# Kernel tuning notes

Hardware: AMD Instinct MI355X
Metric: run time of the kernel (lower is better)

## Reference

```python
import jax, jax.numpy as jnp
import numpy as np
from jax import lax

B, S, IN, H, OUT = 64, 512, 1024, 1024, 512


def setup_inputs() -> dict:
    key = jax.random.key(0)
    ks = jax.random.split(key, 7)
    sc_ih = 1.0 / np.sqrt(IN)
    sc_h = 1.0 / np.sqrt(H)
    return {
        "x": jax.random.normal(ks[0], (B, S, IN), dtype=jnp.float32),
        "w_ih": jax.random.normal(ks[1], (3 * H, IN), dtype=jnp.float32) * sc_ih,
        "w_hh": jax.random.normal(ks[2], (3 * H, H), dtype=jnp.float32) * sc_h,
        "b_ih": jax.random.normal(ks[3], (3 * H,), dtype=jnp.float32) * sc_h,
        "b_hh": jax.random.normal(ks[4], (3 * H,), dtype=jnp.float32) * sc_h,
        "w_out": jax.random.normal(ks[5], (OUT, H), dtype=jnp.float32) * sc_h,
        "b_out": jnp.zeros((OUT,), dtype=jnp.float32),
    }


def reference(x, w_ih, w_hh, b_ih, b_hh, w_out, b_out):
    """x: [B,S,IN] -> [B,S,OUT]. PyTorch GRUCell semantics."""
    Bb, Ss, _ = x.shape
    Hh = w_hh.shape[1]
    # Precompute input-side gate activations for all timesteps: [B,S,3H]
    xg = jnp.einsum("bsi,gi->bsg", x, w_ih) + b_ih
    h0 = jnp.zeros((Bb, Hh), dtype=x.dtype)

    def step(h, xg_t):
        # h: [B,H], xg_t: [B,3H]
        hg = h @ w_hh.T + b_hh  # [B,3H]
        xr, xz, xn = jnp.split(xg_t, 3, axis=-1)
        hr, hz, hn = jnp.split(hg, 3, axis=-1)
        r = jax.nn.sigmoid(xr + hr)
        z = jax.nn.sigmoid(xz + hz)
        n = jnp.tanh(xn + r * hn)
        h_new = (1.0 - z) * n + z * h
        return h_new, h_new

    _, hs = lax.scan(step, h0, jnp.swapaxes(xg, 0, 1))  # hs: [S,B,H]
    hs = jnp.swapaxes(hs, 0, 1)  # [B,S,H]
    return jnp.einsum("bsh,oh->bso", hs, w_out) + b_out
```

## Files before the change

### kernel.cpp

```cpp
#include <hip/hip_runtime.h>
#include <stdint.h>

typedef unsigned int   u32;
typedef unsigned short u16;
typedef __attribute__((ext_vector_type(8))) short bf16x8;
typedef __attribute__((ext_vector_type(4))) float f32x4;

#define DEV __device__ __forceinline__

constexpr int Bsz = 64, Ssz = 512, INsz = 1024, Hsz = 1024, OUTsz = 512;
constexpr int G3 = 3 * Hsz;
constexpr int MR = Bsz * Ssz;
constexpr int TCH = 64;
constexpr int NCH = Ssz / TCH;
constexpr int MCH = Bsz * TCH;

constexpr size_t WHHHI_OFF = 0;
constexpr size_t WHHLO_OFF = WHHHI_OFF + (size_t)G3 * Hsz * 2;
constexpr size_t WIHHI_OFF = WHHLO_OFF + (size_t)G3 * Hsz * 2;
constexpr size_t WIHLO_OFF = WIHHI_OFF + (size_t)G3 * INsz * 2;
constexpr size_t WOHI_OFF  = WIHLO_OFF + (size_t)G3 * INsz * 2;
constexpr size_t WOLO_OFF  = WOHI_OFF  + (size_t)OUTsz * Hsz * 2;
constexpr size_t HS_OFF    = WOLO_OFF  + (size_t)OUTsz * Hsz * 2;
constexpr size_t HP_OFF    = HS_OFF    + (size_t)MR * Hsz * 2;
constexpr size_t HPL       = (size_t)Bsz * Hsz;
constexpr size_t XCHI_OFF  = HP_OFF   + 4 * HPL * 2;
constexpr size_t XCLO_OFF  = XCHI_OFF + (size_t)MCH * INsz * 2;
constexpr size_t XGC_OFF   = XCLO_OFF + (size_t)MCH * INsz * 2;
constexpr size_t WS_TOTAL  = XGC_OFF  + (size_t)MCH * G3 * 4;

DEV u16 f2bf(float f) {
  u32 u = __float_as_uint(f);
  u += 0x7fffu + ((u >> 16) & 1u);
  return (u16)(u >> 16);
}
DEV float bf2f(u16 h) { return __uint_as_float((u32)h << 16); }
DEV void split2(float v, u16& hi, u16& lo) {
  hi = f2bf(v);
  lo = f2bf(v - bf2f(hi));
}

__global__ void diag_ws(float* out, float v) { out[0] = v; }

__global__ void prep_w(const float* __restrict__ wih, const float* __restrict__ whh,
                       const float* __restrict__ wout,
                       u16* __restrict__ wihhi, u16* __restrict__ wihlo,
                       u16* __restrict__ whhhi, u16* __restrict__ whhlo,
                       u16* __restrict__ wohi, u16* __restrict__ wolo) {
  const size_t n1 = (size_t)G3 * INsz;
  const size_t n2 = n1 + (size_t)G3 * Hsz;
  const size_t n3 = n2 + (size_t)OUTsz * Hsz;
  size_t i = (size_t)blockIdx.x * blockDim.x + threadIdx.x;
  const size_t stride = (size_t)gridDim.x * blockDim.x;
  for (; i < n3; i += stride) {
    const float* s; u16 *ph, *pl; size_t j;
    if (i < n1)      { s = wih;  ph = wihhi; pl = wihlo; j = i; }
    else if (i < n2) { s = whh;  ph = whhhi; pl = whhlo; j = i - n1; }
    else             { s = wout; ph = wohi;  pl = wolo;  j = i - n2; }
    u16 hi, lo; split2(s[j], hi, lo);
    ph[j] = hi; pl[j] = lo;
  }
}

__global__ void prep_x(const float* __restrict__ x, int t0,
                       u16* __restrict__ xchi, u16* __restrict__ xclo) {
  const size_t total = (size_t)MCH * INsz;
  size_t i = (size_t)blockIdx.x * blockDim.x + threadIdx.x;
  const size_t stride = (size_t)gridDim.x * blockDim.x;
  for (; i < total; i += stride) {
    const int k = (int)(i & 1023), tc = (int)((i >> 10) & (TCH - 1)), b = (int)(i >> 16);
    const float v = x[((size_t)b * Ssz + t0 + tc) * INsz + k];
    u16 hi, lo; split2(v, hi, lo);
    xchi[i] = hi; xclo[i] = lo;
  }
}

template <bool SPLITA>
__global__ __launch_bounds__(256, 2)
void gemm_ws(const u16* __restrict__ Ahi, const u16* __restrict__ Alo,
             const u16* __restrict__ Bhi, const u16* __restrict__ Blo,
             const float* __restrict__ bias,
             float* __restrict__ C, int M, int N) {
  constexpr int K = 1024;
  constexpr int NT = SPLITA ? 4 : 3;
  __shared__ __align__(16) u16 smem[NT * 128 * 64];
  const int tid = threadIdx.x, lane = tid & 63, wid = tid >> 6;

  int wg = blockIdx.x;
  const int cpx = (int)gridDim.x >> 3;
  wg = (wg & 7) * cpx + (wg >> 3);
  const int NB = N >> 7;
  const int mb = wg / NB, nb = wg % NB;
  const size_t m0 = (size_t)mb * 128, n0 = (size_t)nb * 128;
  const int wm = wid >> 1, wn = wid & 1;

  f32x4 acc[4][4];
#pragma unroll
  for (int i = 0; i < 4; ++i)
#pragma unroll
    for (int j = 0; j < 4; ++j) acc[i][j] = (f32x4)0.f;

  for (int k0 = 0; k0 < K; k0 += 64) {
    __syncthreads();
#pragma unroll
    for (int is = 0; is < NT * 4; ++is) {
      const int g = is * 256 + wid * 64 + lane;
      const int tile = g >> 10;
      const int gi = g & 1023;
      const int row = gi >> 3, gcd = gi & 7;
      const int gcs = gcd ^ (row & 7);
      const u16* src;
      if (SPLITA) {
        if (tile == 0)      src = Ahi + (m0 + row) * K + (k0 + gcs * 8);
        else if (tile == 1) src = Alo + (m0 + row) * K + (k0 + gcs * 8);
        else if (tile == 2) src = Bhi + (n0 + row) * K + (k0 + gcs * 8);
        else                src = Blo + (n0 + row) * K + (k0 + gcs * 8);
      } else {
        if (tile == 0)      src = Ahi + (m0 + row) * K + (k0 + gcs * 8);
        else if (tile == 1) src = Bhi + (n0 + row) * K + (k0 + gcs * 8);
        else                src = Blo + (n0 + row) * K + (k0 + gcs * 8);
      }
      __builtin_amdgcn_global_load_lds(
          (const __attribute__((address_space(1))) void*)src,
          (__attribute__((address_space(3))) void*)&smem[(size_t)(is * 256 + wid * 64) * 8],
          16, 0, 0);
    }
    __syncthreads();

    constexpr int BH_T = SPLITA ? 2 : 1;
#pragma unroll
    for (int kt = 0; kt < 2; ++kt) {
      bf16x8 ah[4], al[4], bh[4], bl[4];
      const int gc = kt * 4 + (lane >> 4);
#pragma unroll
      for (int i = 0; i < 4; ++i) {
        const int row = wm * 64 + i * 16 + (lane & 15);
        const int off = row * 128 + ((gc ^ (row & 7)) << 4);
        ah[i] = *(const bf16x8*)((const char*)smem + off);
        if (SPLITA) al[i] = *(const bf16x8*)((const char*)smem + 16384 + off);
      }
#pragma unroll
      for (int j = 0; j < 4; ++j) {
        const int row = wn * 64 + j * 16 + (lane & 15);
        const int off = row * 128 + ((gc ^ (row & 7)) << 4);
        bh[j] = *(const bf16x8*)((const char*)smem + BH_T * 16384 + off);
        bl[j] = *(const bf16x8*)((const char*)smem + (BH_T + 1) * 16384 + off);
      }
#pragma unroll
      for (int i = 0; i < 4; ++i)
#pragma unroll
        for (int j = 0; j < 4; ++j) {
          acc[i][j] = __builtin_amdgcn_mfma_f32_16x16x32_bf16(ah[i], bh[j], acc[i][j], 0, 0, 0);
          acc[i][j] = __builtin_amdgcn_mfma_f32_16x16x32_bf16(ah[i], bl[j], acc[i][j], 0, 0, 0);
          if (SPLITA)
            acc[i][j] = __builtin_amdgcn_mfma_f32_16x16x32_bf16(al[i], bh[j], acc[i][j], 0, 0, 0);
        }
    }
  }

#pragma unroll
  for (int i = 0; i < 4; ++i) {
    const size_t rbase = m0 + wm * 64 + i * 16 + ((lane >> 4) << 2);
#pragma unroll
    for (int j = 0; j < 4; ++j) {
      const size_t col = n0 + wn * 64 + j * 16 + (lane & 15);
      const float bv = bias[col];
#pragma unroll
      for (int r = 0; r < 4; ++r)
        C[(rbase + r) * (size_t)N + col] = acc[i][j][r] + bv;
    }
  }
}

__global__ __launch_bounds__(256, 2)
void gru_step(const float* __restrict__ xgc, const u16* __restrict__ whhhi,
              const u16* __restrict__ whhlo, const float* __restrict__ bhh,
              int t, int tc,
              const u16* __restrict__ Hhi, const u16* __restrict__ Hlo,
              u16* __restrict__ Nhi, u16* __restrict__ Nlo,
              u16* __restrict__ hs) {
  __shared__ __align__(16) u16 wbuf[2 * 12 * 1024];
  __shared__ float part[64 * 16];

  const int tid = threadIdx.x, lane = tid & 63, wid = tid >> 6;
  const int jc0 = blockIdx.x << 2;

  const int b = tid >> 2, j = tid & 3, col = jc0 + j;
  const size_t xbase = (size_t)(b * TCH + tc) * G3 + col;
  const float xr  = xgc[xbase];
  const float xz  = xgc[xbase + Hsz];
  const float xn_ = xgc[xbase + 2 * Hsz];
  const float bh_r = bhh[col], bh_z = bhh[Hsz + col], bh_n = bhh[2 * Hsz + col];
  const int hidx = b * Hsz + col;
  const float hprev = bf2f(Hhi[hidx]) + bf2f(Hlo[hidx]);

#pragma unroll
  for (int it = 0; it < 12; ++it) {
    const int g = (it % 6) * 256 + tid;
    const int n = g >> 7, gslot = g & 127;
    const int gsrc = gslot ^ (n & 7);
    const int grow = (n >> 2) * Hsz + jc0 + (n & 3);
    const u16* src = (it < 6 ? whhhi : whhlo) + (size_t)grow * Hsz + gsrc * 8;
    u16* dst = wbuf + (it < 6 ? 0 : 12 * 1024) + (size_t)((it % 6) * 256 + wid * 64) * 8;
    __builtin_amdgcn_global_load_lds(
        (const __attribute__((address_space(1))) void*)src,
        (__attribute__((address_space(3))) void*)dst, 16, 0, 0);
  }
  __syncthreads();

  const int mt = wid;
  const int brow = mt * 16 + (lane & 15);
  const int nr = lane & 15;
  const int nc = nr < 12 ? nr : 11;

  f32x4 a_hh = (f32x4)0.f, a_hl = (f32x4)0.f, a_lh = (f32x4)0.f;
#pragma unroll 4
  for (int kt = 0; kt < 32; ++kt) {
    const int koff = (kt << 5) + ((lane >> 4) << 3);
    bf16x8 ahi = *(const bf16x8*)(Hhi + (size_t)brow * Hsz + koff);
    bf16x8 alo = *(const bf16x8*)(Hlo + (size_t)brow * Hsz + koff);
    const int gc = koff >> 3;
    const int boff = (nc << 11) + ((gc ^ (nc & 7)) << 4);
    bf16x8 bhi = *(const bf16x8*)((const char*)wbuf + boff);
    bf16x8 blo = *(const bf16x8*)((const char*)wbuf + 24576 + boff);
    a_hh = __builtin_amdgcn_mfma_f32_16x16x32_bf16(ahi, bhi, a_hh, 0, 0, 0);
    a_hl = __builtin_amdgcn_mfma_f32_16x16x32_bf16(ahi, blo, a_hl, 0, 0, 0);
    a_lh = __builtin_amdgcn_mfma_f32_16x16x32_bf16(alo, bhi, a_lh, 0, 0, 0);
  }
  const f32x4 asum = a_hh + a_hl + a_lh;

  const int r0 = mt * 16 + ((lane >> 4) << 2);
#pragma unroll
  for (int r = 0; r < 4; ++r) part[(r0 + r) * 16 + nr] = asum[r];
  __syncthreads();

  const float hr = part[b * 16 + j] + bh_r;
  const float hz = part[b * 16 + 4 + j] + bh_z;
  const float hn = part[b * 16 + 8 + j] + bh_n;
  const float rr = 1.f / (1.f + expf(-(xr + hr)));
  const float zz = 1.f / (1.f + expf(-(xz + hz)));
  const float nn = tanhf(xn_ + rr * hn);
  const float hnew = (1.f - zz) * nn + zz * hprev;
  u16 hi, lo; split2(hnew, hi, lo);
  Nhi[hidx] = hi; Nlo[hidx] = lo;
  hs[(size_t)(b * Ssz + t) * Hsz + col] = hi;
}

extern "C" void kernel_launch(void* const* d_in, const int* in_sizes, int n_in,
                              void* d_out, int out_size, void* d_ws, size_t ws_size,
                              hipStream_t stream) {
  const float* x     = (const float*)d_in[0];
  const float* w_ih  = (const float*)d_in[1];
  const float* w_hh  = (const float*)d_in[2];
  const float* b_ih  = (const float*)d_in[3];
  const float* b_hh  = (const float*)d_in[4];
  const float* w_out = (const float*)d_in[5];
  const float* b_out = (const float*)d_in[6];
  float* out = (float*)d_out;

  if (ws_size < WS_TOTAL) {
    diag_ws<<<1, 1, 0, stream>>>(out, (float)(ws_size >> 20));
    return;
  }

  char* ws = (char*)d_ws;
  u16* whhhi = (u16*)(ws + WHHHI_OFF);
  u16* whhlo = (u16*)(ws + WHHLO_OFF);
  u16* wihhi = (u16*)(ws + WIHHI_OFF);
  u16* wihlo = (u16*)(ws + WIHLO_OFF);
  u16* wohi  = (u16*)(ws + WOHI_OFF);
  u16* wolo  = (u16*)(ws + WOLO_OFF);
  u16* hsbuf = (u16*)(ws + HS_OFF);
  u16* hp    = (u16*)(ws + HP_OFF);
  u16* h0hi = hp;           u16* h0lo = hp + HPL;
  u16* h1hi = hp + 2 * HPL; u16* h1lo = hp + 3 * HPL;
  u16* xchi  = (u16*)(ws + XCHI_OFF);
  u16* xclo  = (u16*)(ws + XCLO_OFF);
  float* xgc = (float*)(ws + XGC_OFF);

  hipMemsetAsync(h0hi, 0, 2 * HPL * sizeof(u16), stream);

  prep_w<<<2048, 256, 0, stream>>>(w_ih, w_hh, w_out,
                                   wihhi, wihlo, whhhi, whhlo, wohi, wolo);

  for (int c = 0; c < NCH; ++c) {
    prep_x<<<1024, 256, 0, stream>>>(x, c * TCH, xchi, xclo);
    gemm_ws<true><<<768, 256, 0, stream>>>(xchi, xclo, wihhi, wihlo, b_ih, xgc, MCH, G3);
    for (int tcc = 0; tcc < TCH; ++tcc) {
      const int t = c * TCH + tcc;
      const u16* Hh = (t & 1) ? h1hi : h0hi;
      const u16* Hl = (t & 1) ? h1lo : h0lo;
      u16* Nh = (t & 1) ? h0hi : h1hi;
      u16* Nl = (t & 1) ? h0lo : h1lo;
      gru_step<<<256, 256, 0, stream>>>(xgc, whhhi, whhlo, b_hh, t, tcc,
                                        Hh, Hl, Nh, Nl, hsbuf);
    }
  }

  gemm_ws<false><<<1024, 256, 0, stream>>>(hsbuf, nullptr, wohi, wolo, b_out, out, MR, OUTsz);
}
```

Baseline: 7.336 ms.

## Make GRU recurrence a persistent kernel per chunk with grid barriers

Replaces 64 per-timestep gru_step launches per chunk with one persistent gru_scan kernel that loops over the chunk's timesteps. Blocks synchronise through an atomic-counter grid barrier in global memory. Each block loads its W_hh slice into LDS once per chunk instead of once per step, and keeps the hidden state in a register. This removes launch overhead and repeated weight loads. It relies on all 256 blocks being co-resident, since otherwise the spin barrier deadlocks.

```diff
diff --git a/kernel.cpp b/kernel.cpp
--- a/kernel.cpp
+++ b/kernel.cpp
@@ -24,7 +24,8 @@
 constexpr size_t HS_OFF    = WOLO_OFF  + (size_t)OUTsz * Hsz * 2;
 constexpr size_t HP_OFF    = HS_OFF    + (size_t)MR * Hsz * 2;
 constexpr size_t HPL       = (size_t)Bsz * Hsz;
-constexpr size_t XCHI_OFF  = HP_OFF   + 4 * HPL * 2;
+constexpr size_t BAR_OFF   = HP_OFF   + 4 * HPL * 2;
+constexpr size_t XCHI_OFF  = BAR_OFF  + 256;
 constexpr size_t XCLO_OFF  = XCHI_OFF + (size_t)MCH * INsz * 2;
 constexpr size_t XGC_OFF   = XCLO_OFF + (size_t)MCH * INsz * 2;
 constexpr size_t WS_TOTAL  = XGC_OFF  + (size_t)MCH * G3 * 4;
@@ -172,13 +173,25 @@
   }
 }
 
+DEV void grid_bar(u32* cnt, u32 target) {
+  __syncthreads();
+  if (threadIdx.x == 0) {
+    __threadfence();
+    __hip_atomic_fetch_add(cnt, 1u, __ATOMIC_RELAXED, __HIP_MEMORY_SCOPE_AGENT);
+    while (__hip_atomic_load(cnt, __ATOMIC_RELAXED, __HIP_MEMORY_SCOPE_AGENT) < target)
+      __builtin_amdgcn_s_sleep(2);
+    __threadfence();
+  }
+  __syncthreads();
+}
+
 __global__ __launch_bounds__(256, 2)
-void gru_step(const float* __restrict__ xgc, const u16* __restrict__ whhhi,
+void gru_scan(const float* __restrict__ xgc, const u16* __restrict__ whhhi,
               const u16* __restrict__ whhlo, const float* __restrict__ bhh,
-              int t, int tc,
-              const u16* __restrict__ Hhi, const u16* __restrict__ Hlo,
-              u16* __restrict__ Nhi, u16* __restrict__ Nlo,
-              u16* __restrict__ hs) {
+              int t0,
+              u16* __restrict__ h0hi, u16* __restrict__ h0lo,
+              u16* __restrict__ h1hi, u16* __restrict__ h1lo,
+              u16* __restrict__ hs, u32* __restrict__ bar) {
   __shared__ __align__(16) u16 wbuf[2 * 12 * 1024];
   __shared__ float part[64 * 16];
 
@@ -186,13 +199,8 @@
   const int jc0 = blockIdx.x << 2;
 
   const int b = tid >> 2, j = tid & 3, col = jc0 + j;
-  const size_t xbase = (size_t)(b * TCH + tc) * G3 + col;
-  const float xr  = xgc[xbase];
-  const float xz  = xgc[xbase + Hsz];
-  const float xn_ = xgc[xbase + 2 * Hsz];
   const float bh_r = bhh[col], bh_z = bhh[Hsz + col], bh_n = bhh[2 * Hsz + col];
   const int hidx = b * Hsz + col;
-  const float hprev = bf2f(Hhi[hidx]) + bf2f(Hlo[hidx]);
 
 #pragma unroll
   for (int it = 0; it < 12; ++it) {
@@ -208,42 +216,70 @@
   }
   __syncthreads();
 
+  float hstate;
+  {
+    const u16* Hi = (t0 & 1) ? h1hi : h0hi;
+    const u16* Lo = (t0 & 1) ? h1lo : h0lo;
+    hstate = bf2f(Hi[hidx]) + bf2f(Lo[hidx]);
+  }
+
   const int mt = wid;
   const int brow = mt * 16 + (lane & 15);
   const int nr = lane & 15;
   const int nc = nr < 12 ? nr : 11;
 
-  f32x4 a_hh = (f32x4)0.f, a_hl = (f32x4)0.f, a_lh = (f32x4)0.f;
+  float xr, xz, xn_;
+  {
+    const size_t xb = (size_t)(b * TCH) * G3 + col;
+    xr = xgc[xb]; xz = xgc[xb + Hsz]; xn_ = xgc[xb + 2 * Hsz];
+  }
+
+  for (int tc = 0; tc < TCH; ++tc) {
+    const int t = t0 + tc;
+    const u16* Hhi = (t & 1) ? h1hi : h0hi;
+    const u16* Hlo = (t & 1) ? h1lo : h0lo;
+    u16* Nhi = (t & 1) ? h0hi : h1hi;
+    u16* Nlo = (t & 1) ? h0lo : h1lo;
+
+    f32x4 a_hh = (f32x4)0.f, a_hl = (f32x4)0.f, a_lh = (f32x4)0.f;
 #pragma unroll 4
-  for (int kt = 0; kt < 32; ++kt) {
-    const int koff = (kt << 5) + ((lane >> 4) << 3);
-    bf16x8 ahi = *(const bf16x8*)(Hhi + (size_t)brow * Hsz + koff);
-    bf16x8 alo = *(const bf16x8*)(Hlo + (size_t)brow * Hsz + koff);
-    const int gc = koff >> 3;
-    const int boff = (nc << 11) + ((gc ^ (nc & 7)) << 4);
-    bf16x8 bhi = *(const bf16x8*)((const char*)wbuf + boff);
-    bf16x8 blo = *(const bf16x8*)((const char*)wbuf + 24576 + boff);
-    a_hh = __builtin_amdgcn_mfma_f32_16x16x32_bf16(ahi, bhi, a_hh, 0, 0, 0);
-    a_hl = __builtin_amdgcn_mfma_f32_16x16x32_bf16(ahi, blo, a_hl, 0, 0, 0);
-    a_lh = __builtin_amdgcn_mfma_f32_16x16x32_bf16(alo, bhi, a_lh, 0, 0, 0);
-  }
-  const f32x4 asum = a_hh + a_hl + a_lh;
-
-  const int r0 = mt * 16 + ((lane >> 4) << 2);
-#pragma unroll
-  for (int r = 0; r < 4; ++r) part[(r0 + r) * 16 + nr] = asum[r];
-  __syncthreads();
-
-  const float hr = part[b * 16 + j] + bh_r;
-  const float hz = part[b * 16 + 4 + j] + bh_z;
-  const float hn = part[b * 16 + 8 + j] + bh_n;
-  const float rr = 1.f / (1.f + expf(-(xr + hr)));
-  const float zz = 1.f / (1.f + expf(-(xz + hz)));
-  const float nn = tanhf(xn_ + rr * hn);
-  const float hnew = (1.f - zz) * nn + zz * hprev;
-  u16 hi, lo; split2(hnew, hi, lo);
-  Nhi[hidx] = hi; Nlo[hidx] = lo;
-  hs[(size_t)(b * Ssz + t) * Hsz + col] = hi;
+    for (int kt = 0; kt < 32; ++kt) {
+      const int koff = (kt << 5) + ((lane >> 4) << 3);
+      bf16x8 ahi = *(const bf16x8*)(Hhi + (size_t)brow * Hsz + koff);
+      bf16x8 alo = *(const bf16x8*)(Hlo + (size_t)brow * Hsz + koff);
+      const int gc = koff >> 3;
+      const int boff = (nc << 11) + ((gc ^ (nc & 7)) << 4);
+      bf16x8 bhi = *(const bf16x8*)((const char*)wbuf + boff);
+      bf16x8 blo = *(const bf16x8*)((const char*)wbuf + 24576 + boff);
+      a_hh = __builtin_amdgcn_mfma_f32_16x16x32_bf16(ahi, bhi, a_hh, 0, 0, 0);
+      a_hl = __builtin_amdgcn_mfma_f32_16x16x32_bf16(ahi, blo, a_hl, 0, 0, 0);
+      a_lh = __builtin_amdgcn_mfma_f32_16x16x32_bf16(alo, bhi, a_lh, 0, 0, 0);
+    }
+    const f32x4 asum = a_hh + a_hl + a_lh;
+
+    const int r0 = mt * 16 + ((lane >> 4) << 2);
+#pragma unroll
+    for (int r = 0; r < 4; ++r) part[(r0 + r) * 16 + nr] = asum[r];
+    __syncthreads();
+
+    const float hr = part[b * 16 + j] + bh_r;
+    const float hz = part[b * 16 + 4 + j] + bh_z;
+    const float hn = part[b * 16 + 8 + j] + bh_n;
+    const float rr = 1.f / (1.f + expf(-(xr + hr)));
+    const float zz = 1.f / (1.f + expf(-(xz + hz)));
+    const float nn = tanhf(xn_ + rr * hn);
+    const float hnew = (1.f - zz) * nn + zz * hstate;
+    hstate = hnew;
+    u16 hi, lo; split2(hnew, hi, lo);
+    Nhi[hidx] = hi; Nlo[hidx] = lo;
+    hs[(size_t)(b * Ssz + t) * Hsz + col] = hi;
+
+    if (tc + 1 < TCH) {
+      const size_t xb = (size_t)(b * TCH + tc + 1) * G3 + col;
+      xr = xgc[xb]; xz = xgc[xb + Hsz]; xn_ = xgc[xb + 2 * Hsz];
+      grid_bar(bar, 256u * (u32)(tc + 1));
+    }
+  }
 }
 
 extern "C" void kernel_launch(void* const* d_in, const int* in_sizes, int n_in,
@@ -274,6 +310,7 @@
   u16* hp    = (u16*)(ws + HP_OFF);
   u16* h0hi = hp;           u16* h0lo = hp + HPL;
   u16* h1hi = hp + 2 * HPL; u16* h1lo = hp + 3 * HPL;
+  u32* bar   = (u32*)(ws + BAR_OFF);
   u16* xchi  = (u16*)(ws + XCHI_OFF);
   u16* xclo  = (u16*)(ws + XCLO_OFF);
   float* xgc = (float*)(ws + XGC_OFF);
@@ -286,15 +323,9 @@
   for (int c = 0; c < NCH; ++c) {
     prep_x<<<1024, 256, 0, stream>>>(x, c * TCH, xchi, xclo);
     gemm_ws<true><<<768, 256, 0, stream>>>(xchi, xclo, wihhi, wihlo, b_ih, xgc, MCH, G3);
-    for (int tcc = 0; tcc < TCH; ++tcc) {
-      const int t = c * TCH + tcc;
-      const u16* Hh = (t & 1) ? h1hi : h0hi;
-      const u16* Hl = (t & 1) ? h1lo : h0lo;
-      u16* Nh = (t & 1) ? h0hi : h1hi;
-      u16* Nl = (t & 1) ? h0lo : h1lo;
-      gru_step<<<256, 256, 0, stream>>>(xgc, whhhi, whhlo, b_hh, t, tcc,
-                                        Hh, Hl, Nh, Nl, hsbuf);
-    }
+    hipMemsetAsync(bar, 0, sizeof(u32), stream);
+    gru_scan<<<256, 256, 0, stream>>>(xgc, whhhi, whhlo, b_hh, c * TCH,
+                                      h0hi, h0lo, h1hi, h1lo, hsbuf, bar);
   }
 
   gemm_ws<false><<<1024, 256, 0, stream>>>(hsbuf, nullptr, wohi, wolo, b_out, out, MR, OUTsz);
```

Result: slower. 18.03 ms (+145.8%).
